# Performance work log

Measured on AMD Instinct MI355X. Metric: run time of the kernel, lower is better.

## Reference

```python
import jax, jax.numpy as jnp
import numpy as np

N_NODES = 50000
EPS = 1e-5


def sage_conv_max(x, src, dst, W_l, b_l, W_r):
    # PyG SAGEConv(aggr='max'): out = lin_l(max_j x_j) + lin_r(x_i)
    msg = x[src]                                   # [E, d] gather
    agg = jnp.full((x.shape[0], x.shape[1]), -jnp.inf, dtype=x.dtype)
    agg = agg.at[dst].max(msg)                     # scatter-max over edges
    agg = jnp.where(jnp.isneginf(agg), 0.0, agg)   # isolated nodes -> 0 (PyG convention)
    return agg @ W_l.T + b_l + x @ W_r.T


def batch_norm(x, gamma, beta):
    mean = jnp.mean(x, axis=0)
    var = jnp.var(x, axis=0)
    return (x - mean) * jax.lax.rsqrt(var + EPS) * gamma + beta


def setup_inputs() -> dict:
    key = jax.random.key(0)
    ks = jax.random.split(key, 10)
    d_in, d_h, d_out = 128, 128, 32
    s = lambda fan: 1.0 / np.sqrt(fan)
    return {
        "x": jax.random.normal(ks[0], (N_NODES, d_in), dtype=jnp.float32),
        "edge_index": jax.random.randint(ks[1], (2, 800000), 0, N_NODES, dtype=jnp.int32),
        "W_l1": jax.random.uniform(ks[2], (d_h, d_in), jnp.float32, -s(d_in), s(d_in)),
        "b_l1": jnp.zeros((d_h,), jnp.float32),
        "W_r1": jax.random.uniform(ks[3], (d_h, d_in), jnp.float32, -s(d_in), s(d_in)),
        "gamma1": jnp.ones((d_h,), jnp.float32),
        "beta1": jnp.zeros((d_h,), jnp.float32),
        "W_l2": jax.random.uniform(ks[4], (d_out, d_h), jnp.float32, -s(d_h), s(d_h)),
        "b_l2": jnp.zeros((d_out,), jnp.float32),
        "W_r2": jax.random.uniform(ks[5], (d_out, d_h), jnp.float32, -s(d_h), s(d_h)),
    }


def reference(x, edge_index, W_l1, b_l1, W_r1, gamma1, beta1, W_l2, b_l2, W_r2):
    src, dst = edge_index[0], edge_index[1]
    h = sage_conv_max(x, src, dst, W_l1, b_l1, W_r1)
    h = batch_norm(h, gamma1, beta1)
    h = jax.nn.relu(h)
    # dropout is identity at inference
    return sage_conv_max(h, src, dst, W_l2, b_l2, W_r2)
```

## Files before the change

### kernel.cpp

```cpp
#include <hip/hip_runtime.h>
#include <math.h>
#include <float.h>

#define N_NODES 50000
#define N_EDGES 800000
#define NB 392
#define EB 2048
#define NBUCK 196
#define BSH 8
#define CAP 36
#define SEGC 4864
#define CELLS_PER_BUCKET (NB * CAP)

typedef __attribute__((ext_vector_type(8))) short bf16x8;
typedef __attribute__((ext_vector_type(4))) float f32x4;

static __device__ __forceinline__ unsigned short f2bf(float f) {
  unsigned int u = __float_as_uint(f);
  u = (u + 0x7fff + ((u >> 16) & 1)) >> 16;
  return (unsigned short)u;
}

__global__ __launch_bounds__(256) void setup_kernel(
    const int* __restrict__ src, const int* __restrict__ dst,
    unsigned int* __restrict__ pairs, int* __restrict__ counts,
    const float* __restrict__ x, const float* __restrict__ Wl1,
    const float* __restrict__ Wr1, const float* __restrict__ Wl2,
    const float* __restrict__ Wr2, unsigned int* __restrict__ x_bf,
    unsigned short* __restrict__ Wcat1, unsigned short* __restrict__ Wcat2,
    float* __restrict__ gsums) {
  const int b = blockIdx.x, tid = threadIdx.x;
  if (b < NB) {
    __shared__ int cur[NBUCK];
    if (tid < NBUCK) cur[tid] = 0;
    __syncthreads();
#pragma unroll
    for (int it = 0; it < EB / 256; ++it) {
      int e = b * EB + it * 256 + tid;
      if (e < N_EDGES) {
        int d = dst[e];
        int bk = d >> BSH;
        int p = atomicAdd(&cur[bk], 1);
        if (p < CAP)
          pairs[(size_t)(bk * NB + b) * CAP + p] =
              (unsigned)src[e] | ((unsigned)(d & 255) << 16);
      }
    }
    __syncthreads();
    if (tid < NBUCK) {
      int c = cur[tid];
      counts[tid * NB + b] = c > CAP ? CAP : c;
    }
  } else if (b < NB + 6250) {
    int i = (b - NB) * 256 + tid;
    float4 v = ((const float4*)x)[i];
    uint2 o;
    o.x = (unsigned int)f2bf(v.x) | ((unsigned int)f2bf(v.y) << 16);
    o.y = (unsigned int)f2bf(v.z) | ((unsigned int)f2bf(v.w) << 16);
    ((uint2*)x_bf)[i] = o;
  } else if (b < NB + 6410) {
    int i = (b - NB - 6250) * 256 + tid;
    if (i < 32768) {
      int n = i >> 8, k = i & 255;
      float w = (k < 128) ? Wl1[n * 128 + k] : Wr1[n * 128 + (k - 128)];
      Wcat1[i] = f2bf(w);
    } else if (i < 40960) {
      int j = i - 32768;
      int n = j >> 8, k = j & 255;
      float w = (k < 128) ? Wl2[n * 128 + k] : Wr2[n * 128 + (k - 128)];
      Wcat2[j] = f2bf(w);
    }
  } else {
#pragma unroll
    for (int i = 0; i < 8; ++i) gsums[i * 256 + tid] = 0.f;
  }
}

__global__ __launch_bounds__(1024) void bucket_sort(const unsigned int* __restrict__ pairs,
                                                    const int* __restrict__ counts,
                                                    unsigned int* __restrict__ rowinfo,
                                                    int* __restrict__ elist) {
  __shared__ int hist[256], cpos[256], cnt[NB];
  __shared__ int wsum[4];
  const int b = blockIdx.x, tid = threadIdx.x;
  const size_t s0 = (size_t)b * CELLS_PER_BUCKET;
  if (tid < 256) hist[tid] = 0;
  if (tid < NB) cnt[tid] = counts[b * NB + tid];
  __syncthreads();
  for (int p = tid; p < CELLS_PER_BUCKET; p += 1024) {
    int c = p / CAP, s = p - c * CAP;
    if (s < cnt[c]) {
      unsigned int pr = pairs[s0 + p];
      atomicAdd(&hist[(pr >> 16) & 255], 1);
    }
  }
  __syncthreads();
  int incl = 0, h = 0;
  if (tid < 256) {
    const int l = tid & 63;
    h = hist[tid];
    incl = h;
#pragma unroll
    for (int off = 1; off < 64; off <<= 1) {
      int t = __shfl_up(incl, off, 64);
      if (l >= off) incl += t;
    }
    if (l == 63) wsum[tid >> 6] = incl;
  }
  __syncthreads();
  if (tid < 64) {
    int v = (tid < 4) ? wsum[tid] : 0;
#pragma unroll
    for (int off = 1; off < 4; off <<= 1) {
      int t = __shfl_up(v, off, 64);
      if (tid >= off) v += t;
    }
    if (tid < 4) wsum[tid] = v;
  }
  __syncthreads();
  if (tid < 256) {
    const int w = tid >> 6;
    int tot = incl + ((w > 0) ? wsum[w - 1] : 0);
    int excl = tot - h;
    cpos[tid] = excl;
    int node = (b << BSH) + tid;
    if (node < N_NODES)
      rowinfo[node] = (unsigned)(b * SEGC + excl) | ((unsigned)h << 20);
  }
  __syncthreads();
  for (int p = tid; p < CELLS_PER_BUCKET; p += 1024) {
    int c = p / CAP, s = p - c * CAP;
    if (s < cnt[c]) {
      unsigned int pr = pairs[s0 + p];
      int loc = atomicAdd(&cpos[(pr >> 16) & 255], 1);
      elist[b * SEGC + loc] = (int)(pr & 0xffffu);
    }
  }
}

template <bool BN>
__global__ __launch_bounds__(256) void agg_max_bf16(const uint4* __restrict__ feat4,
                                                    const unsigned int* __restrict__ rowinfo,
                                                    const int* __restrict__ elist,
                                                    const float* __restrict__ gsums,
                                                    const float* __restrict__ gamma,
                                                    const float* __restrict__ beta,
                                                    uint4* __restrict__ out4) {
  __shared__ float s_scale[128], s_shift[128];
  if (BN) {
    int t = threadIdx.x;
    if (t < 128) {
      float sm = 0.f, sq = 0.f;
#pragma unroll
      for (int r = 0; r < 8; ++r) {
        sm += gsums[r * 256 + t];
        sq += gsums[r * 256 + 128 + t];
      }
      const float inv = 1.f / (float)N_NODES;
      float mean = sm * inv;
      float var = sq * inv - mean * mean;
      float sc = gamma[t] * rsqrtf(var + 1e-5f);
      s_scale[t] = sc;
      s_shift[t] = beta[t] - mean * sc;
    }
    __syncthreads();
  }

  int node = blockIdx.x * 4 + (threadIdx.x >> 6);
  int lane = threadIdx.x & 63;
  int eslot = lane >> 4;
  int fq = lane & 15;
  unsigned int info = rowinfo[node];
  int e0 = (int)(info & 0xFFFFFu);
  int deg = (int)(info >> 20);
  int e1 = e0 + deg;
  float m[8];
#pragma unroll
  for (int j = 0; j < 8; ++j) m[j] = -FLT_MAX;

  if (deg > 0) {
    const int last = e1 - 1;
    for (int base = e0; base < e1; base += 16) {
      int idx[4];
#pragma unroll
      for (int q = 0; q < 4; ++q) {
        int e = base + q * 4 + eslot;
        if (e > last) e = last;
        idx[q] = elist[e];
      }
      uint4 v[4];
#pragma unroll
      for (int q = 0; q < 4; ++q) v[q] = feat4[(size_t)idx[q] * 16 + fq];
#pragma unroll
      for (int q = 0; q < 4; ++q) {
        const unsigned int* pv = (const unsigned int*)&v[q];
#pragma unroll
        for (int c = 0; c < 4; ++c) {
          m[2 * c]     = fmaxf(m[2 * c],     __uint_as_float(pv[c] << 16));
          m[2 * c + 1] = fmaxf(m[2 * c + 1], __uint_as_float(pv[c] & 0xffff0000u));
        }
      }
    }
  }

#pragma unroll
  for (int j = 0; j < 8; ++j) {
    m[j] = fmaxf(m[j], __shfl_xor(m[j], 16, 64));
    m[j] = fmaxf(m[j], __shfl_xor(m[j], 32, 64));
  }
  if (eslot == 0) {
    if (deg == 0) {
#pragma unroll
      for (int j = 0; j < 8; ++j) m[j] = 0.f;
    } else if (BN) {
#pragma unroll
      for (int j = 0; j < 8; ++j) {
        int col = fq * 8 + j;
        m[j] = fmaxf(m[j] * s_scale[col] + s_shift[col], 0.f);
      }
    }
    uint4 o;
    o.x = (unsigned)f2bf(m[0]) | ((unsigned)f2bf(m[1]) << 16);
    o.y = (unsigned)f2bf(m[2]) | ((unsigned)f2bf(m[3]) << 16);
    o.z = (unsigned)f2bf(m[4]) | ((unsigned)f2bf(m[5]) << 16);
    o.w = (unsigned)f2bf(m[6]) | ((unsigned)f2bf(m[7]) << 16);
    out4[(size_t)node * 16 + fq] = o;
  }
}

template <bool COLSPLIT, int LDO, bool BF16OUT, bool STATS, bool BNIN>
__global__ __launch_bounds__(256) void gemm_breg(
    const unsigned short* __restrict__ Aa, const unsigned short* __restrict__ Ab,
    const unsigned short* __restrict__ Wcat, const float* __restrict__ bias,
    unsigned short* __restrict__ outb, float* __restrict__ outf,
    float* __restrict__ gsums, const float* __restrict__ gamma,
    const float* __restrict__ beta, int N) {
  __shared__ float s_sum[128], s_sq[128];
  __shared__ float s_scale[128], s_shift[128];
  const int tid = threadIdx.x;

  if (STATS && tid < 128) { s_sum[tid] = 0.f; s_sq[tid] = 0.f; }
  if (BNIN && tid < 128) {
    float sm = 0.f, sq = 0.f;
#pragma unroll
    for (int r = 0; r < 8; ++r) {
      sm += gsums[r * 256 + tid];
      sq += gsums[r * 256 + 128 + tid];
    }
    const float inv = 1.f / (float)N_NODES;
    float mean = sm * inv;
    float var = sq * inv - mean * mean;
    float sc = gamma[tid] * rsqrtf(var + 1e-5f);
    s_scale[tid] = sc;
    s_shift[tid] = beta[tid] - mean * sc;
  }
  if (STATS || BNIN) __syncthreads();

  const int wv = tid >> 6;
  const int lane = tid & 63;
  const int ln15 = lane & 15;
  const int quad = lane >> 4;
  const int ct0 = COLSPLIT ? wv * 2 : 0;
  const int rowBase = COLSPLIT ? blockIdx.x * 64
                               : blockIdx.x * 256 + wv * 64;

  bf16x8 breg[8][2];
#pragma unroll
  for (int ks = 0; ks < 8; ++ks) {
    const int off = ks * 32 + quad * 8;
#pragma unroll
    for (int j = 0; j < 2; ++j)
      breg[ks][j] = *(const bf16x8*)(Wcat + (size_t)((ct0 + j) * 16 + ln15) * 256 + off);
  }

  float psum[2] = {0.f, 0.f}, psq[2] = {0.f, 0.f};

#pragma unroll
  for (int s = 0; s < 4; ++s) {
    const int mrow = rowBase + s * 16;
    int r0 = mrow + ln15;
    if (r0 >= N) r0 = N - 1;
    bf16x8 a[8];
#pragma unroll
    for (int ks = 0; ks < 8; ++ks) {
      const int off = ks * 32 + quad * 8;
      if (ks < 4) {
        a[ks] = *(const bf16x8*)(Aa + (size_t)r0 * 128 + off);
      } else {
        const int kb = off - 128;
        a[ks] = *(const bf16x8*)(Ab + (size_t)r0 * 128 + kb);
        if (BNIN) {
          unsigned int* p = (unsigned int*)&a[ks];
#pragma unroll
          for (int c = 0; c < 4; ++c) {
            int k = kb + 2 * c;
            float lo = __uint_as_float(p[c] << 16);
            float hi = __uint_as_float(p[c] & 0xffff0000u);
            lo = fmaxf(lo * s_scale[k] + s_shift[k], 0.f);
            hi = fmaxf(hi * s_scale[k + 1] + s_shift[k + 1], 0.f);
            p[c] = (unsigned)f2bf(lo) | ((unsigned)f2bf(hi) << 16);
          }
        }
      }
    }
    f32x4 acc[2] = {};
#pragma unroll
    for (int ks = 0; ks < 8; ++ks)
#pragma unroll
      for (int j = 0; j < 2; ++j)
        acc[j] = __builtin_amdgcn_mfma_f32_16x16x32_bf16(a[ks], breg[ks][j], acc[j], 0, 0, 0);
#pragma unroll
    for (int j = 0; j < 2; ++j) {
      int col = (ct0 + j) * 16 + ln15;
      float bv = bias[col];
#pragma unroll
      for (int i = 0; i < 4; ++i) {
        int r = mrow + quad * 4 + i;
        if (r < N) {
          float val = acc[j][i] + bv;
          if (STATS) { psum[j] += val; psq[j] += val * val; }
          if (BF16OUT)
            outb[(size_t)r * LDO + col] = f2bf(val);
          else
            outf[(size_t)r * LDO + col] = val;
        }
      }
    }
  }

  if (STATS) {
#pragma unroll
    for (int j = 0; j < 2; ++j) {
      int col = (ct0 + j) * 16 + ln15;
      atomicAdd(&s_sum[col], psum[j]);
      atomicAdd(&s_sq[col], psq[j]);
    }
    __syncthreads();
    if (tid < 128) {
      int rep = blockIdx.x & 7;
      atomicAdd(&gsums[rep * 256 + tid], s_sum[tid]);
      atomicAdd(&gsums[rep * 256 + 128 + tid], s_sq[tid]);
    }
  }
}

extern "C" void kernel_launch(void* const* d_in, const int* in_sizes, int n_in,
                              void* d_out, int out_size, void* d_ws, size_t ws_size,
                              hipStream_t stream) {
  (void)in_sizes; (void)n_in; (void)out_size; (void)ws_size;
  const float* x     = (const float*)d_in[0];
  const int*   eidx  = (const int*)d_in[1];
  const float* W_l1  = (const float*)d_in[2];
  const float* b_l1  = (const float*)d_in[3];
  const float* W_r1  = (const float*)d_in[4];
  const float* gamma = (const float*)d_in[5];
  const float* beta  = (const float*)d_in[6];
  const float* W_l2  = (const float*)d_in[7];
  const float* b_l2  = (const float*)d_in[8];
  const float* W_r2  = (const float*)d_in[9];
  const int* srcp = eidx;
  const int* dstp = eidx + N_EDGES;
  float* out = (float*)d_out;

  int* wsi = (int*)d_ws;
  float* gsums   = (float*)wsi;
  unsigned int* rowinfo = (unsigned int*)(wsi + 2048);
  int*   counts  = wsi + 52224;
  int*   elist   = wsi + 129056;
  unsigned int* pairs   = (unsigned int*)(wsi + 1082400);
  unsigned int* x_bf    = (unsigned int*)(wsi + 3848352);
  unsigned int* agg_bf  = (unsigned int*)(wsi + 7048352);
  unsigned int* h_bf    = (unsigned int*)(wsi + 10248352);
  unsigned short* Wcat1 = (unsigned short*)(wsi + 13448352);
  unsigned short* Wcat2 = (unsigned short*)(wsi + 13464736);

  setup_kernel<<<dim3(NB + 6410 + 1), 256, 0, stream>>>(
      srcp, dstp, pairs, counts, x, W_l1, W_r1, W_l2, W_r2, x_bf, Wcat1, Wcat2, gsums);

  bucket_sort<<<dim3(NBUCK), 1024, 0, stream>>>(pairs, counts, rowinfo, elist);

  agg_max_bf16<false><<<dim3(N_NODES / 4), 256, 0, stream>>>(
      (const uint4*)x_bf, rowinfo, elist, nullptr, nullptr, nullptr, (uint4*)agg_bf);
  gemm_breg<true, 128, true, true, false><<<dim3(784), 256, 0, stream>>>(
      (const unsigned short*)agg_bf, (const unsigned short*)x_bf, Wcat1, b_l1,
      (unsigned short*)h_bf, nullptr, gsums, nullptr, nullptr, N_NODES);

  agg_max_bf16<true><<<dim3(N_NODES / 4), 256, 0, stream>>>(
      (const uint4*)h_bf, rowinfo, elist, gsums, gamma, beta, (uint4*)agg_bf);
  gemm_breg<false, 32, false, false, true><<<dim3(196), 256, 0, stream>>>(
      (const unsigned short*)agg_bf, (const unsigned short*)h_bf, Wcat2, b_l2,
      nullptr, out, gsums, gamma, beta, N_NODES);
}
```

Before: 205.7 us.

## Fuse neighbor max-aggregation with GEMM per layer via shared-memory A tile

Merges the separate aggregation and GEMM kernels into one fused_layer kernel per layer. Each 64-row block gathers and max-reduces its neighbor features into an LDS tile, stages the self-features next to them, then runs the MFMA GEMM straight from LDS. This drops the agg_bf round trip through global memory and two kernel launches. In exchange, each wave now walks 16 nodes one after another, and the large LDS tile may lower occupancy for the latency-bound gather.

```diff
diff --git a/kernel.cpp b/kernel.cpp
--- a/kernel.cpp
+++ b/kernel.cpp
@@ -11,6 +11,7 @@
 #define CAP 36
 #define SEGC 4864
 #define CELLS_PER_BUCKET (NB * CAP)
+#define FBLK 782
 
 typedef __attribute__((ext_vector_type(8))) short bf16x8;
 typedef __attribute__((ext_vector_type(4))) float f32x4;
@@ -138,132 +139,134 @@
   }
 }
 
-template <bool BN>
-__global__ __launch_bounds__(256) void agg_max_bf16(const uint4* __restrict__ feat4,
-                                                    const unsigned int* __restrict__ rowinfo,
-                                                    const int* __restrict__ elist,
-                                                    const float* __restrict__ gsums,
-                                                    const float* __restrict__ gamma,
-                                                    const float* __restrict__ beta,
-                                                    uint4* __restrict__ out4) {
-  __shared__ float s_scale[128], s_shift[128];
-  if (BN) {
-    int t = threadIdx.x;
-    if (t < 128) {
-      float sm = 0.f, sq = 0.f;
-#pragma unroll
-      for (int r = 0; r < 8; ++r) {
-        sm += gsums[r * 256 + t];
-        sq += gsums[r * 256 + 128 + t];
-      }
-      const float inv = 1.f / (float)N_NODES;
-      float mean = sm * inv;
-      float var = sq * inv - mean * mean;
-      float sc = gamma[t] * rsqrtf(var + 1e-5f);
-      s_scale[t] = sc;
-      s_shift[t] = beta[t] - mean * sc;
-    }
-    __syncthreads();
-  }
-
-  int node = blockIdx.x * 4 + (threadIdx.x >> 6);
-  int lane = threadIdx.x & 63;
-  int eslot = lane >> 4;
-  int fq = lane & 15;
-  unsigned int info = rowinfo[node];
-  int e0 = (int)(info & 0xFFFFFu);
-  int deg = (int)(info >> 20);
-  int e1 = e0 + deg;
-  float m[8];
-#pragma unroll
-  for (int j = 0; j < 8; ++j) m[j] = -FLT_MAX;
-
-  if (deg > 0) {
-    const int last = e1 - 1;
-    for (int base = e0; base < e1; base += 16) {
-      int idx[4];
-#pragma unroll
-      for (int q = 0; q < 4; ++q) {
-        int e = base + q * 4 + eslot;
-        if (e > last) e = last;
-        idx[q] = elist[e];
-      }
-      uint4 v[4];
-#pragma unroll
-      for (int q = 0; q < 4; ++q) v[q] = feat4[(size_t)idx[q] * 16 + fq];
-#pragma unroll
-      for (int q = 0; q < 4; ++q) {
-        const unsigned int* pv = (const unsigned int*)&v[q];
-#pragma unroll
-        for (int c = 0; c < 4; ++c) {
-          m[2 * c]     = fmaxf(m[2 * c],     __uint_as_float(pv[c] << 16));
-          m[2 * c + 1] = fmaxf(m[2 * c + 1], __uint_as_float(pv[c] & 0xffff0000u));
-        }
-      }
-    }
-  }
-
-#pragma unroll
-  for (int j = 0; j < 8; ++j) {
-    m[j] = fmaxf(m[j], __shfl_xor(m[j], 16, 64));
-    m[j] = fmaxf(m[j], __shfl_xor(m[j], 32, 64));
-  }
-  if (eslot == 0) {
-    if (deg == 0) {
-#pragma unroll
-      for (int j = 0; j < 8; ++j) m[j] = 0.f;
-    } else if (BN) {
-#pragma unroll
-      for (int j = 0; j < 8; ++j) {
-        int col = fq * 8 + j;
-        m[j] = fmaxf(m[j] * s_scale[col] + s_shift[col], 0.f);
-      }
-    }
-    uint4 o;
-    o.x = (unsigned)f2bf(m[0]) | ((unsigned)f2bf(m[1]) << 16);
-    o.y = (unsigned)f2bf(m[2]) | ((unsigned)f2bf(m[3]) << 16);
-    o.z = (unsigned)f2bf(m[4]) | ((unsigned)f2bf(m[5]) << 16);
-    o.w = (unsigned)f2bf(m[6]) | ((unsigned)f2bf(m[7]) << 16);
-    out4[(size_t)node * 16 + fq] = o;
-  }
-}
-
-template <bool COLSPLIT, int LDO, bool BF16OUT, bool STATS, bool BNIN>
-__global__ __launch_bounds__(256) void gemm_breg(
-    const unsigned short* __restrict__ Aa, const unsigned short* __restrict__ Ab,
+#define ASTR 264
+
+template <int NCOLT, int LDO, bool BF16OUT, bool STATS, bool BN>
+__global__ __launch_bounds__(256) void fused_layer(
+    const uint4* __restrict__ feat4,
+    const unsigned short* __restrict__ Ab,
+    const unsigned int* __restrict__ rowinfo,
+    const int* __restrict__ elist,
     const unsigned short* __restrict__ Wcat, const float* __restrict__ bias,
     unsigned short* __restrict__ outb, float* __restrict__ outf,
     float* __restrict__ gsums, const float* __restrict__ gamma,
     const float* __restrict__ beta, int N) {
+  __shared__ unsigned short Alds[64 * ASTR];
   __shared__ float s_sum[128], s_sq[128];
   __shared__ float s_scale[128], s_shift[128];
   const int tid = threadIdx.x;
+  const int rowBase = blockIdx.x * 64;
 
   if (STATS && tid < 128) { s_sum[tid] = 0.f; s_sq[tid] = 0.f; }
-  if (BNIN && tid < 128) {
-    float sm = 0.f, sq = 0.f;
-#pragma unroll
-    for (int r = 0; r < 8; ++r) {
-      sm += gsums[r * 256 + tid];
-      sq += gsums[r * 256 + 128 + tid];
-    }
-    const float inv = 1.f / (float)N_NODES;
-    float mean = sm * inv;
-    float var = sq * inv - mean * mean;
-    float sc = gamma[tid] * rsqrtf(var + 1e-5f);
-    s_scale[tid] = sc;
-    s_shift[tid] = beta[tid] - mean * sc;
-  }
-  if (STATS || BNIN) __syncthreads();
+  if (BN) {
+    if (tid < 128) {
+      float sm = 0.f, sq = 0.f;
+#pragma unroll
+      for (int r = 0; r < 8; ++r) {
+        sm += gsums[r * 256 + tid];
+        sq += gsums[r * 256 + 128 + tid];
+      }
+      const float inv = 1.f / (float)N_NODES;
+      float mean = sm * inv;
+      float var = sq * inv - mean * mean;
+      float sc = gamma[tid] * rsqrtf(var + 1e-5f);
+      s_scale[tid] = sc;
+      s_shift[tid] = beta[tid] - mean * sc;
+    }
+    __syncthreads();
+  }
+
+#pragma unroll
+  for (int it = 0; it < 4; ++it) {
+    int f = tid + it * 256;
+    int r = f >> 4, seg = f & 15;
+    int n = rowBase + r;
+    if (n >= N) n = N - 1;
+    int4 d = *(const int4*)(Ab + (size_t)n * 128 + seg * 8);
+    if (BN) {
+      int kb = seg * 8;
+      unsigned int* dp = (unsigned int*)&d;
+#pragma unroll
+      for (int c = 0; c < 4; ++c) {
+        int k0 = kb + 2 * c;
+        float lo = __uint_as_float(dp[c] << 16);
+        float hi = __uint_as_float(dp[c] & 0xffff0000u);
+        lo = fmaxf(lo * s_scale[k0] + s_shift[k0], 0.f);
+        hi = fmaxf(hi * s_scale[k0 + 1] + s_shift[k0 + 1], 0.f);
+        dp[c] = (unsigned)f2bf(lo) | ((unsigned)f2bf(hi) << 16);
+      }
+    }
+    *(int4*)(&Alds[r * ASTR + 128 + seg * 8]) = d;
+  }
 
   const int wv = tid >> 6;
   const int lane = tid & 63;
+  const int eslot = lane >> 4;
+  const int fq = lane & 15;
+  for (int it = 0; it < 16; ++it) {
+    int r = wv * 16 + it;
+    int node = rowBase + r;
+    if (node >= N) node = N - 1;
+    unsigned int info = rowinfo[node];
+    int e0 = (int)(info & 0xFFFFFu);
+    int deg = (int)(info >> 20);
+    int e1 = e0 + deg;
+    float m[8];
+#pragma unroll
+    for (int j = 0; j < 8; ++j) m[j] = -FLT_MAX;
+    if (deg > 0) {
+      const int last = e1 - 1;
+      for (int base = e0; base < e1; base += 16) {
+        int idx[4];
+#pragma unroll
+        for (int q = 0; q < 4; ++q) {
+          int e = base + q * 4 + eslot;
+          if (e > last) e = last;
+          idx[q] = elist[e];
+        }
+        uint4 v[4];
+#pragma unroll
+        for (int q = 0; q < 4; ++q) v[q] = feat4[(size_t)idx[q] * 16 + fq];
+#pragma unroll
+        for (int q = 0; q < 4; ++q) {
+          const unsigned int* pv = (const unsigned int*)&v[q];
+#pragma unroll
+          for (int c = 0; c < 4; ++c) {
+            m[2 * c]     = fmaxf(m[2 * c],     __uint_as_float(pv[c] << 16));
+            m[2 * c + 1] = fmaxf(m[2 * c + 1], __uint_as_float(pv[c] & 0xffff0000u));
+          }
+        }
+      }
+    }
+#pragma unroll
+    for (int j = 0; j < 8; ++j) {
+      m[j] = fmaxf(m[j], __shfl_xor(m[j], 16, 64));
+      m[j] = fmaxf(m[j], __shfl_xor(m[j], 32, 64));
+    }
+    if (eslot == 0) {
+      if (deg == 0) {
+#pragma unroll
+        for (int j = 0; j < 8; ++j) m[j] = 0.f;
+      } else if (BN) {
+#pragma unroll
+        for (int j = 0; j < 8; ++j) {
+          int col = fq * 8 + j;
+          m[j] = fmaxf(m[j] * s_scale[col] + s_shift[col], 0.f);
+        }
+      }
+      int4 o;
+      unsigned int* op = (unsigned int*)&o;
+      op[0] = (unsigned)f2bf(m[0]) | ((unsigned)f2bf(m[1]) << 16);
+      op[1] = (unsigned)f2bf(m[2]) | ((unsigned)f2bf(m[3]) << 16);
+      op[2] = (unsigned)f2bf(m[4]) | ((unsigned)f2bf(m[5]) << 16);
+      op[3] = (unsigned)f2bf(m[6]) | ((unsigned)f2bf(m[7]) << 16);
+      *(int4*)(&Alds[r * ASTR + fq * 8]) = o;
+    }
+  }
+
   const int ln15 = lane & 15;
   const int quad = lane >> 4;
-  const int ct0 = COLSPLIT ? wv * 2 : 0;
-  const int rowBase = COLSPLIT ? blockIdx.x * 64
-                               : blockIdx.x * 256 + wv * 64;
-
+  const int ct0 = (NCOLT == 8) ? wv * 2 : 0;
   bf16x8 breg[8][2];
 #pragma unroll
   for (int ks = 0; ks < 8; ++ks) {
@@ -272,37 +275,20 @@
     for (int j = 0; j < 2; ++j)
       breg[ks][j] = *(const bf16x8*)(Wcat + (size_t)((ct0 + j) * 16 + ln15) * 256 + off);
   }
+  __syncthreads();
 
   float psum[2] = {0.f, 0.f}, psq[2] = {0.f, 0.f};
-
-#pragma unroll
-  for (int s = 0; s < 4; ++s) {
-    const int mrow = rowBase + s * 16;
-    int r0 = mrow + ln15;
-    if (r0 >= N) r0 = N - 1;
+  const int S0 = (NCOLT == 8) ? 0 : wv;
+  const int SN = (NCOLT == 8) ? 4 : 1;
+#pragma unroll
+  for (int si = 0; si < 4; ++si) {
+    if (si >= SN) break;
+    const int s = S0 + si;
+    const int mrow = s * 16;
     bf16x8 a[8];
 #pragma unroll
-    for (int ks = 0; ks < 8; ++ks) {
-      const int off = ks * 32 + quad * 8;
-      if (ks < 4) {
-        a[ks] = *(const bf16x8*)(Aa + (size_t)r0 * 128 + off);
-      } else {
-        const int kb = off - 128;
-        a[ks] = *(const bf16x8*)(Ab + (size_t)r0 * 128 + kb);
-        if (BNIN) {
-          unsigned int* p = (unsigned int*)&a[ks];
-#pragma unroll
-          for (int c = 0; c < 4; ++c) {
-            int k = kb + 2 * c;
-            float lo = __uint_as_float(p[c] << 16);
-            float hi = __uint_as_float(p[c] & 0xffff0000u);
-            lo = fmaxf(lo * s_scale[k] + s_shift[k], 0.f);
-            hi = fmaxf(hi * s_scale[k + 1] + s_shift[k + 1], 0.f);
-            p[c] = (unsigned)f2bf(lo) | ((unsigned)f2bf(hi) << 16);
-          }
-        }
-      }
-    }
+    for (int ks = 0; ks < 8; ++ks)
+      a[ks] = *(const bf16x8*)(&Alds[(mrow + ln15) * ASTR + ks * 32 + quad * 8]);
     f32x4 acc[2] = {};
 #pragma unroll
     for (int ks = 0; ks < 8; ++ks)
@@ -315,7 +301,7 @@
       float bv = bias[col];
 #pragma unroll
       for (int i = 0; i < 4; ++i) {
-        int r = mrow + quad * 4 + i;
+        int r = rowBase + mrow + quad * 4 + i;
         if (r < N) {
           float val = acc[j][i] + bv;
           if (STATS) { psum[j] += val; psq[j] += val * val; }
@@ -369,7 +355,6 @@
   int*   elist   = wsi + 129056;
   unsigned int* pairs   = (unsigned int*)(wsi + 1082400);
   unsigned int* x_bf    = (unsigned int*)(wsi + 3848352);
-  unsigned int* agg_bf  = (unsigned int*)(wsi + 7048352);
   unsigned int* h_bf    = (unsigned int*)(wsi + 10248352);
   unsigned short* Wcat1 = (unsigned short*)(wsi + 13448352);
   unsigned short* Wcat2 = (unsigned short*)(wsi + 13464736);
@@ -379,15 +364,11 @@
 
   bucket_sort<<<dim3(NBUCK), 1024, 0, stream>>>(pairs, counts, rowinfo, elist);
 
-  agg_max_bf16<false><<<dim3(N_NODES / 4), 256, 0, stream>>>(
-      (const uint4*)x_bf, rowinfo, elist, nullptr, nullptr, nullptr, (uint4*)agg_bf);
-  gemm_breg<true, 128, true, true, false><<<dim3(784), 256, 0, stream>>>(
-      (const unsigned short*)agg_bf, (const unsigned short*)x_bf, Wcat1, b_l1,
+  fused_layer<8, 128, true, true, false><<<dim3(FBLK), 256, 0, stream>>>(
+      (const uint4*)x_bf, (const unsigned short*)x_bf, rowinfo, elist, Wcat1, b_l1,
       (unsigned short*)h_bf, nullptr, gsums, nullptr, nullptr, N_NODES);
 
-  agg_max_bf16<true><<<dim3(N_NODES / 4), 256, 0, stream>>>(
-      (const uint4*)h_bf, rowinfo, elist, gsums, gamma, beta, (uint4*)agg_bf);
-  gemm_breg<false, 32, false, false, true><<<dim3(196), 256, 0, stream>>>(
-      (const unsigned short*)agg_bf, (const unsigned short*)h_bf, Wcat2, b_l2,
+  fused_layer<2, 32, false, false, true><<<dim3(FBLK), 256, 0, stream>>>(
+      (const uint4*)h_bf, (const unsigned short*)h_bf, rowinfo, elist, Wcat2, b_l2,
       nullptr, out, gsums, gamma, beta, N_NODES);
 }
```

New measurement: 213.9 us. 1.04x slower.
